# Kernel tuning notes

Measured on AMD Instinct MI355X. Metric: run time of the kernel, lower is better.

Reference implementation:

```python
import jax, jax.numpy as jnp
import numpy as np

HEADS = 12
HEAD_SIZE = 64

def sinusoidal(L, d, dtype):
    # bert4keras SinusoidalPositionEmbedding: interleaved [sin, cos] pairs
    pos = jnp.arange(L, dtype=dtype)
    freqs = 10000.0 ** (-jnp.arange(0, d, 2, dtype=dtype) / d)  # [d/2]
    ang = pos[:, None] * freqs[None, :]                          # [L, d/2]
    return jnp.stack([jnp.sin(ang), jnp.cos(ang)], axis=-1).reshape(L, d)

def rope(x, sin2, cos2):
    # interleaved rotation: pairs (x0,x1) -> (x0*cos - x1*sin, x1*cos + x0*sin)
    x2 = jnp.stack([-x[..., 1::2], x[..., ::2]], axis=-1).reshape(x.shape)
    return x * cos2 + x2 * sin2

def setup_inputs() -> dict:
    key = jax.random.key(0)
    ks = jax.random.split(key, 3)
    B, L, D = 2, 2048, 768
    x = jax.random.normal(ks[0], (B, L, D), jnp.float32)
    pW = jax.random.normal(ks[1], (D, 2 * HEAD_SIZE), jnp.float32) / np.sqrt(D).astype(np.float32)
    pb = jnp.zeros((2 * HEAD_SIZE,), jnp.float32)
    qW = jax.random.normal(ks[2], (2 * HEAD_SIZE, 2 * HEADS), jnp.float32) / np.sqrt(2 * HEAD_SIZE).astype(np.float32)
    qb = jnp.zeros((2 * HEADS,), jnp.float32)
    return {"x": x, "pW": pW, "pb": pb, "qW": qW, "qb": qb}

def reference(x, pW, pb, qW, qb):
    B, L, _ = x.shape
    h = x @ pW + pb                                   # [B, L, 2*head_size]
    qw, kw = h[..., ::2], h[..., 1::2]                # [B, L, head_size] each
    pos = sinusoidal(L, HEAD_SIZE, x.dtype)           # [L, head_size]
    cos2 = jnp.repeat(pos[..., 1::2], 2, axis=-1)     # [L, head_size]
    sin2 = jnp.repeat(pos[..., ::2], 2, axis=-1)
    qw = rope(qw, sin2, cos2)
    kw = rope(kw, sin2, cos2)
    logits = jnp.einsum('bmd,bnd->bmn', qw, kw) / HEAD_SIZE ** 0.5  # [B, L, L]
    bias = jnp.transpose(h @ qW + qb, (0, 2, 1)) / 2.0              # [B, 2*heads, L]
    # [B, heads, L, L]
    logits = logits[:, None] + bias[:, ::2, None, :] + bias[:, 1::2, :, None]
    tril = jnp.triu(jnp.ones((L, L), bool))
    return jnp.where(tril, logits, -jnp.inf)
```

## Files before the change

### kernel.cpp

```cpp
#include <hip/hip_runtime.h>
#include <math.h>

#define SEQ 2048
#define DIM 768
#define NH  12
#define HS  64

#define MASK_VAL (-3.0e38f)

typedef float f32x4 __attribute__((ext_vector_type(4)));

__global__ __launch_bounds__(256) void k_prep(
    const float* __restrict__ x, const float* __restrict__ pW,
    const float* __restrict__ pb, const float* __restrict__ qW,
    const float* __restrict__ qb,
    float* __restrict__ qwv, float* __restrict__ kwv, float* __restrict__ biasv)
{
    __shared__ float hs[16][132];
    const int t = threadIdx.x;
    const int row0 = blockIdx.x * 16;
    const int cg = t & 31;
    const int rg = t >> 5;
    const int c4 = cg * 4;

    float acc[2][4];
    #pragma unroll
    for (int j = 0; j < 4; ++j) { float pv = pb[c4 + j]; acc[0][j] = pv; acc[1][j] = pv; }

    const float* xr0 = x + (size_t)(row0 + rg * 2) * DIM;
    const float* xr1 = xr0 + DIM;

    #pragma unroll 2
    for (int k4 = 0; k4 < DIM / 4; ++k4) {
        float4 a0 = *(const float4*)(xr0 + k4 * 4);
        float4 a1 = *(const float4*)(xr1 + k4 * 4);
        float a0v[4] = {a0.x, a0.y, a0.z, a0.w};
        float a1v[4] = {a1.x, a1.y, a1.z, a1.w};
        #pragma unroll
        for (int kk = 0; kk < 4; ++kk) {
            float4 w = *(const float4*)(pW + (size_t)(k4 * 4 + kk) * 128 + c4);
            float wv[4] = {w.x, w.y, w.z, w.w};
            #pragma unroll
            for (int j = 0; j < 4; ++j) {
                acc[0][j] = fmaf(a0v[kk], wv[j], acc[0][j]);
                acc[1][j] = fmaf(a1v[kk], wv[j], acc[1][j]);
            }
        }
    }
    #pragma unroll
    for (int r = 0; r < 2; ++r)
        *(float4*)(&hs[rg * 2 + r][c4]) = make_float4(acc[r][0], acc[r][1], acc[r][2], acc[r][3]);
    __syncthreads();

    for (int idx = t; idx < 16 * 24; idx += 256) {
        int r = idx / 24, c = idx - (idx / 24) * 24;
        float a = qb[c];
        #pragma unroll 4
        for (int k = 0; k < 128; ++k) a = fmaf(hs[r][k], qW[k * 24 + c], a);
        int grow = row0 + r;
        int b = grow >> 11, l = grow & (SEQ - 1);
        biasv[((size_t)b * 24 + c) * SEQ + l] = a * 0.5f;
    }

    for (int idx = t; idx < 16 * 32; idx += 256) {
        int r = idx >> 5, i = idx & 31;
        int grow = row0 + r;
        int l = grow & (SEQ - 1);
        float freq = (float)pow(10000.0, -(double)(2 * i) / 64.0);
        float ang = (float)l * freq;
        float s = sinf(ang), c = cosf(ang);
        float4 hq = *(const float4*)(&hs[r][4 * i]);
        size_t o = (size_t)grow * HS + 2 * i;
        *(float2*)(qwv + o) = make_float2(hq.x * c - hq.z * s, hq.z * c + hq.x * s);
        *(float2*)(kwv + o) = make_float2(hq.y * c - hq.w * s, hq.w * c + hq.y * s);
    }
}

__global__ __launch_bounds__(256, 4) void k_logits(
    const float* __restrict__ qwv, const float* __restrict__ kwv,
    const float* __restrict__ biasv, float* __restrict__ out)
{
    const int nt = blockIdx.x, mt = blockIdx.y, b = blockIdx.z;
    const int t = threadIdx.x;
    const int tn = t & 15, tm = t >> 4;
    const int m0 = mt * 64, n0 = nt * 64;
    float* outb = out + (size_t)b * NH * SEQ * SEQ;

    if (mt > nt) {
        const f32x4 ninf = {MASK_VAL, MASK_VAL, MASK_VAL, MASK_VAL};
        #pragma unroll
        for (int h = 0; h < NH; ++h) {
            float* plane = outb + (size_t)h * SEQ * SEQ;
            #pragma unroll
            for (int rr = 0; rr < 4; ++rr) {
                int m = m0 + rr * 16 + tm;
                __builtin_nontemporal_store(ninf,
                    (f32x4*)(plane + (size_t)m * SEQ + n0 + tn * 4));
            }
        }
        return;
    }

    __shared__ float qwT[64][68];
    __shared__ float kwT[64][68];
    __shared__ float bAs[NH][64];
    __shared__ float bBs[NH][64];

    {
        const float* qg = qwv + ((size_t)b * SEQ + m0) * HS;
        const float* kg = kwv + ((size_t)b * SEQ + n0) * HS;
        #pragma unroll
        for (int it = 0; it < 4; ++it) {
            int row = it * 16 + (t >> 4);
            int d4 = (t & 15) * 4;
            float4 vq = *(const float4*)(qg + row * HS + d4);
            float4 vk = *(const float4*)(kg + row * HS + d4);
            qwT[d4 + 0][row] = vq.x; qwT[d4 + 1][row] = vq.y;
            qwT[d4 + 2][row] = vq.z; qwT[d4 + 3][row] = vq.w;
            kwT[d4 + 0][row] = vk.x; kwT[d4 + 1][row] = vk.y;
            kwT[d4 + 2][row] = vk.z; kwT[d4 + 3][row] = vk.w;
        }
        #pragma unroll
        for (int it = 0; it < 3; ++it) {
            int idx = t + it * 256;
            int h = idx >> 6, j = idx & 63;
            bAs[h][j] = biasv[((size_t)b * 24 + 2 * h    ) * SEQ + n0 + j];
            bBs[h][j] = biasv[((size_t)b * 24 + 2 * h + 1) * SEQ + m0 + j];
        }
    }
    __syncthreads();

    float acc[4][4] = {};
    #pragma unroll 4
    for (int k = 0; k < 64; ++k) {
        float4 aq = *(const float4*)(&qwT[k][tm * 4]);
        float4 ak = *(const float4*)(&kwT[k][tn * 4]);
        float aqv[4] = {aq.x, aq.y, aq.z, aq.w};
        float akv[4] = {ak.x, ak.y, ak.z, ak.w};
        #pragma unroll
        for (int i = 0; i < 4; ++i)
            #pragma unroll
            for (int j = 0; j < 4; ++j)
                acc[i][j] = fmaf(aqv[i], akv[j], acc[i][j]);
    }

    const bool diag = (mt == nt);
    #pragma unroll
    for (int h = 0; h < NH; ++h) {
        float4 ba = *(const float4*)(&bAs[h][tn * 4]);
        float bav[4] = {ba.x, ba.y, ba.z, ba.w};
        float* plane = outb + (size_t)h * SEQ * SEQ;
        #pragma unroll
        for (int i = 0; i < 4; ++i) {
            int m = m0 + tm * 4 + i;
            float bb = bBs[h][tm * 4 + i];
            f32x4 v;
            #pragma unroll
            for (int j = 0; j < 4; ++j)
                v[j] = fmaf(acc[i][j], 0.125f, bav[j] + bb);
            if (diag) {
                int nbase = n0 + tn * 4;
                #pragma unroll
                for (int j = 0; j < 4; ++j)
                    if (m > nbase + j) v[j] = MASK_VAL;
            }
            __builtin_nontemporal_store(v,
                (f32x4*)(plane + (size_t)m * SEQ + n0 + tn * 4));
        }
    }
}

extern "C" void kernel_launch(void* const* d_in, const int* in_sizes, int n_in,
                              void* d_out, int out_size, void* d_ws, size_t ws_size,
                              hipStream_t stream) {
    const float* x  = (const float*)d_in[0];
    const float* pW = (const float*)d_in[1];
    const float* pb = (const float*)d_in[2];
    const float* qW = (const float*)d_in[3];
    const float* qb = (const float*)d_in[4];
    float* out = (float*)d_out;

    float* ws    = (float*)d_ws;
    float* qwv   = ws;
    float* kwv   = ws + 2 * SEQ * HS;
    float* biasv = ws + 4 * SEQ * HS;

    k_prep  <<<dim3(256),        dim3(256), 0, stream>>>(x, pW, pb, qW, qb, qwv, kwv, biasv);
    k_logits<<<dim3(32, 32, 2),  dim3(256), 0, stream>>>(qwv, kwv, biasv, out);
}
```

Measured before the change: 150.5 us.

## Split logits into QK GEMM kernel and row-streaming bias/mask output kernel

Computes the scaled Q·K product once per batch into a workspace buffer, then a separate streaming kernel adds the per-head biases, applies the causal mask and writes full contiguous output rows. This aims to get fully coalesced, row-wise output stores and to decouple the GEMM from the large write phase. It adds an extra write and read of a 2×2048×2048 intermediate and an extra launch. It falls back to the fused kernel if the workspace is too small.

```diff
diff --git a/kernel.cpp b/kernel.cpp
--- a/kernel.cpp
+++ b/kernel.cpp
@@ -76,36 +76,18 @@
     }
 }
 
-__global__ __launch_bounds__(256, 4) void k_logits(
+__global__ __launch_bounds__(256) void k_qk(
     const float* __restrict__ qwv, const float* __restrict__ kwv,
-    const float* __restrict__ biasv, float* __restrict__ out)
+    float* __restrict__ qk)
 {
     const int nt = blockIdx.x, mt = blockIdx.y, b = blockIdx.z;
+    if (mt > nt) return;
     const int t = threadIdx.x;
     const int tn = t & 15, tm = t >> 4;
     const int m0 = mt * 64, n0 = nt * 64;
-    float* outb = out + (size_t)b * NH * SEQ * SEQ;
-
-    if (mt > nt) {
-        const f32x4 ninf = {MASK_VAL, MASK_VAL, MASK_VAL, MASK_VAL};
-        #pragma unroll
-        for (int h = 0; h < NH; ++h) {
-            float* plane = outb + (size_t)h * SEQ * SEQ;
-            #pragma unroll
-            for (int rr = 0; rr < 4; ++rr) {
-                int m = m0 + rr * 16 + tm;
-                __builtin_nontemporal_store(ninf,
-                    (f32x4*)(plane + (size_t)m * SEQ + n0 + tn * 4));
-            }
-        }
-        return;
-    }
 
     __shared__ float qwT[64][68];
     __shared__ float kwT[64][68];
-    __shared__ float bAs[NH][64];
-    __shared__ float bBs[NH][64];
-
     {
         const float* qg = qwv + ((size_t)b * SEQ + m0) * HS;
         const float* kg = kwv + ((size_t)b * SEQ + n0) * HS;
@@ -120,6 +102,124 @@
             kwT[d4 + 0][row] = vk.x; kwT[d4 + 1][row] = vk.y;
             kwT[d4 + 2][row] = vk.z; kwT[d4 + 3][row] = vk.w;
         }
+    }
+    __syncthreads();
+
+    float acc[4][4] = {};
+    #pragma unroll 4
+    for (int k = 0; k < 64; ++k) {
+        float4 aq = *(const float4*)(&qwT[k][tm * 4]);
+        float4 ak = *(const float4*)(&kwT[k][tn * 4]);
+        float aqv[4] = {aq.x, aq.y, aq.z, aq.w};
+        float akv[4] = {ak.x, ak.y, ak.z, ak.w};
+        #pragma unroll
+        for (int i = 0; i < 4; ++i)
+            #pragma unroll
+            for (int j = 0; j < 4; ++j)
+                acc[i][j] = fmaf(aqv[i], akv[j], acc[i][j]);
+    }
+
+    float* qkb = qk + (size_t)b * SEQ * SEQ;
+    #pragma unroll
+    for (int i = 0; i < 4; ++i) {
+        int m = m0 + tm * 4 + i;
+        f32x4 v = { acc[i][0] * 0.125f, acc[i][1] * 0.125f,
+                    acc[i][2] * 0.125f, acc[i][3] * 0.125f };
+        *(f32x4*)(qkb + (size_t)m * SEQ + n0 + tn * 4) = v;
+    }
+}
+
+__global__ __launch_bounds__(256) void k_out(
+    const float* __restrict__ qk, const float* __restrict__ biasv,
+    float* __restrict__ out)
+{
+    const int t = threadIdx.x;
+    const int lane = t & 63;
+    const int wid = blockIdx.x * 4 + (t >> 6);
+    const int mg = wid & 511;
+    const int h  = (wid >> 9) % NH;
+    const int b  = wid / (512 * NH);
+    const int l4 = lane * 4;
+
+    const float* qkrow0 = qk + (size_t)b * SEQ * SEQ;
+    const float* bArow  = biasv + ((size_t)b * 24 + 2 * h) * SEQ;
+    const float* bBrow  = biasv + ((size_t)b * 24 + 2 * h + 1) * SEQ;
+    float* plane = out + (((size_t)b * NH + h) * SEQ) * SEQ;
+    const f32x4 mask4 = {MASK_VAL, MASK_VAL, MASK_VAL, MASK_VAL};
+
+    #pragma unroll
+    for (int i = 0; i < 4; ++i) {
+        const int m = mg * 4 + i;
+        const float* qkrow = qkrow0 + (size_t)m * SEQ;
+        float* orow = plane + (size_t)m * SEQ;
+        const float bB = bBrow[m];
+
+        #pragma unroll
+        for (int c = 0; c < 8; ++c) {
+            const int cm = c * 256;
+            f32x4 v;
+            if (cm + 255 < m) {
+                v = mask4;
+            } else {
+                f32x4 q4 = *(const f32x4*)(qkrow + cm + l4);
+                f32x4 a4 = *(const f32x4*)(bArow + cm + l4);
+                v = q4 + a4;
+                v += bB;
+                if (cm < m) {
+                    int nn = cm + l4;
+                    #pragma unroll
+                    for (int j = 0; j < 4; ++j)
+                        if (nn + j < m) v[j] = MASK_VAL;
+                }
+            }
+            __builtin_nontemporal_store(v, (f32x4*)(orow + cm + l4));
+        }
+    }
+}
+
+__global__ __launch_bounds__(256, 4) void k_logits_fused(
+    const float* __restrict__ qwv, const float* __restrict__ kwv,
+    const float* __restrict__ biasv, float* __restrict__ out)
+{
+    const int nt = blockIdx.x, mt = blockIdx.y, b = blockIdx.z;
+    const int t = threadIdx.x;
+    const int tn = t & 15, tm = t >> 4;
+    const int m0 = mt * 64, n0 = nt * 64;
+    float* outb = out + (size_t)b * NH * SEQ * SEQ;
+
+    if (mt > nt) {
+        const f32x4 ninf = {MASK_VAL, MASK_VAL, MASK_VAL, MASK_VAL};
+        #pragma unroll
+        for (int h = 0; h < NH; ++h) {
+            float* plane = outb + (size_t)h * SEQ * SEQ;
+            #pragma unroll
+            for (int rr = 0; rr < 4; ++rr) {
+                int m = m0 + rr * 16 + tm;
+                __builtin_nontemporal_store(ninf,
+                    (f32x4*)(plane + (size_t)m * SEQ + n0 + tn * 4));
+            }
+        }
+        return;
+    }
+
+    __shared__ float qwT[64][68];
+    __shared__ float kwT[64][68];
+    __shared__ float bAs[NH][64];
+    __shared__ float bBs[NH][64];
+    {
+        const float* qg = qwv + ((size_t)b * SEQ + m0) * HS;
+        const float* kg = kwv + ((size_t)b * SEQ + n0) * HS;
+        #pragma unroll
+        for (int it = 0; it < 4; ++it) {
+            int row = it * 16 + (t >> 4);
+            int d4 = (t & 15) * 4;
+            float4 vq = *(const float4*)(qg + row * HS + d4);
+            float4 vk = *(const float4*)(kg + row * HS + d4);
+            qwT[d4 + 0][row] = vq.x; qwT[d4 + 1][row] = vq.y;
+            qwT[d4 + 2][row] = vq.z; qwT[d4 + 3][row] = vq.w;
+            kwT[d4 + 0][row] = vk.x; kwT[d4 + 1][row] = vk.y;
+            kwT[d4 + 2][row] = vk.z; kwT[d4 + 3][row] = vk.w;
+        }
         #pragma unroll
         for (int it = 0; it < 3; ++it) {
             int idx = t + it * 256;
@@ -184,7 +284,16 @@
     float* qwv   = ws;
     float* kwv   = ws + 2 * SEQ * HS;
     float* biasv = ws + 4 * SEQ * HS;
-
-    k_prep  <<<dim3(256),        dim3(256), 0, stream>>>(x, pW, pb, qW, qb, qwv, kwv, biasv);
-    k_logits<<<dim3(32, 32, 2),  dim3(256), 0, stream>>>(qwv, kwv, biasv, out);
-}
+    float* qkws  = ws + 4 * SEQ * HS + 2 * 24 * SEQ;
+    const size_t need = ((size_t)4 * SEQ * HS + 2 * 24 * SEQ
+                         + (size_t)2 * SEQ * SEQ) * sizeof(float);
+
+    k_prep<<<dim3(256), dim3(256), 0, stream>>>(x, pW, pb, qW, qb, qwv, kwv, biasv);
+
+    if (ws_size >= need) {
+        k_qk <<<dim3(32, 32, 2), dim3(256), 0, stream>>>(qwv, kwv, qkws);
+        k_out<<<dim3(3072),      dim3(256), 0, stream>>>(qkws, biasv, out);
+    } else {
+        k_logits_fused<<<dim3(32, 32, 2), dim3(256), 0, stream>>>(qwv, kwv, biasv, out);
+    }
+}
```

Result: slower. 171.6 us (+14.0%).

## Split masked-region fill into a separate row-contiguous kernel before logits

Applied to the files above, without the earlier changes.

Adds a dedicated fill kernel that writes the mask value row by row for all columns below the diagonal, one wavefront per output row. The logits kernel then returns at once for fully masked tiles and only computes the live upper-triangular tiles. The aim is to turn the masked stores into long contiguous row writes instead of scattered 64-column tile segments, and to stop the masked tiles from taking up logits blocks. The cost is an extra kernel launch, uneven work per wavefront, plain stores in place of nontemporal ones, some duplicate writes inside diagonal tiles, and dropping the occupancy hint on the live kernel.

```diff
diff --git a/kernel.cpp b/kernel.cpp
--- a/kernel.cpp
+++ b/kernel.cpp
@@ -76,36 +76,47 @@
     }
 }
 
-__global__ __launch_bounds__(256, 4) void k_logits(
+__global__ __launch_bounds__(256) void k_fill_masked(float* __restrict__ out)
+{
+    const int lane = threadIdx.x & 63;
+    const int wid  = blockIdx.x * 4 + (threadIdx.x >> 6);
+    const int m  = wid & (SEQ - 1);
+    const int hh = (wid >> 11) % NH;
+    const int b  = wid / (SEQ * NH);
+    if (m == 0) return;
+
+    float* row = out + (((size_t)b * NH + hh) * SEQ + m) * SEQ;
+    const f32x4 mv = {MASK_VAL, MASK_VAL, MASK_VAL, MASK_VAL};
+
+    const int nfull = m >> 8;
+    for (int c = 0; c < nfull; ++c)
+        *(f32x4*)(row + c * 256 + lane * 4) = mv;
+
+    const int base = nfull * 256 + lane * 4;
+    if (base + 3 < m) {
+        *(f32x4*)(row + base) = mv;
+    } else {
+        #pragma unroll
+        for (int j = 0; j < 4; ++j)
+            if (base + j < m) row[base + j] = MASK_VAL;
+    }
+}
+
+__global__ __launch_bounds__(256) void k_live(
     const float* __restrict__ qwv, const float* __restrict__ kwv,
     const float* __restrict__ biasv, float* __restrict__ out)
 {
     const int nt = blockIdx.x, mt = blockIdx.y, b = blockIdx.z;
+    if (mt > nt) return;
     const int t = threadIdx.x;
     const int tn = t & 15, tm = t >> 4;
     const int m0 = mt * 64, n0 = nt * 64;
     float* outb = out + (size_t)b * NH * SEQ * SEQ;
 
-    if (mt > nt) {
-        const f32x4 ninf = {MASK_VAL, MASK_VAL, MASK_VAL, MASK_VAL};
-        #pragma unroll
-        for (int h = 0; h < NH; ++h) {
-            float* plane = outb + (size_t)h * SEQ * SEQ;
-            #pragma unroll
-            for (int rr = 0; rr < 4; ++rr) {
-                int m = m0 + rr * 16 + tm;
-                __builtin_nontemporal_store(ninf,
-                    (f32x4*)(plane + (size_t)m * SEQ + n0 + tn * 4));
-            }
-        }
-        return;
-    }
-
     __shared__ float qwT[64][68];
     __shared__ float kwT[64][68];
     __shared__ float bAs[NH][64];
     __shared__ float bBs[NH][64];
-
     {
         const float* qg = qwv + ((size_t)b * SEQ + m0) * HS;
         const float* kg = kwv + ((size_t)b * SEQ + n0) * HS;
@@ -185,6 +196,7 @@
     float* kwv   = ws + 2 * SEQ * HS;
     float* biasv = ws + 4 * SEQ * HS;
 
-    k_prep  <<<dim3(256),        dim3(256), 0, stream>>>(x, pW, pb, qW, qb, qwv, kwv, biasv);
-    k_logits<<<dim3(32, 32, 2),  dim3(256), 0, stream>>>(qwv, kwv, biasv, out);
-}
+    k_fill_masked<<<dim3(12288),     dim3(256), 0, stream>>>(out);
+    k_prep       <<<dim3(256),       dim3(256), 0, stream>>>(x, pW, pb, qW, qb, qwv, kwv, biasv);
+    k_live       <<<dim3(32, 32, 2), dim3(256), 0, stream>>>(qwv, kwv, biasv, out);
+}
```

Result: slower. 162.7 us (+8.1%).
